# Kernel optimization log

Measured on AMD Instinct MI355X. Metric: run time of the kernel, lower is better.

Reference implementation:

```python
import jax, jax.numpy as jnp
from jax import lax
import numpy as np

N = 87296
NUM_CLASSES = 91
IOU_THRESH = 0.6
MAX_OUT = 100
IMG = 2048.0


def setup_inputs() -> dict:
    key = jax.random.key(0)
    k1, k2, k3, k4, k5 = jax.random.split(key, 5)
    class_logits = jax.random.normal(k1, (N, NUM_CLASSES), dtype=jnp.float32)
    box_regression = jax.random.normal(k2, (N, 4), dtype=jnp.float32)
    box_ctrness = jax.random.normal(k3, (N, 1), dtype=jnp.float32)
    # anchors: valid x1,y1,x2,y2 boxes inside a 2048x2048 image
    ctr = jax.random.uniform(k4, (N, 2), dtype=jnp.float32) * IMG
    wh = jax.random.uniform(k5, (N, 2), dtype=jnp.float32) * 64.0 + 8.0
    anchors = jnp.concatenate([ctr - 0.5 * wh, ctr + 0.5 * wh], axis=1)
    return {"class_logits": class_logits, "box_regression": box_regression,
            "box_ctrness": box_ctrness, "anchors": anchors}


def _decode(rel_codes, anchors):
    # torchvision BoxLinearCoder(normalize_by_size=True).decode
    ctr_x = 0.5 * (anchors[:, 0] + anchors[:, 2])
    ctr_y = 0.5 * (anchors[:, 1] + anchors[:, 3])
    w = anchors[:, 2] - anchors[:, 0]
    h = anchors[:, 3] - anchors[:, 1]
    dl = rel_codes[:, 0] * w
    dt = rel_codes[:, 1] * h
    dr = rel_codes[:, 2] * w
    db = rel_codes[:, 3] * h
    return jnp.stack([ctr_x - dl, ctr_y - dt, ctr_x + dr, ctr_y + db], axis=1)


def _nms_keep(boxes, scores, iou_thresh, max_out):
    # torchvision.ops.nms truncated to max_out; returns indices sorted by score.
    areas = jnp.maximum(boxes[:, 2] - boxes[:, 0], 0.0) * jnp.maximum(boxes[:, 3] - boxes[:, 1], 0.0)

    def body(i, state):
        cur_scores, keep = state
        idx = jnp.argmax(cur_scores)
        keep = keep.at[i].set(idx.astype(jnp.int32))
        b = boxes[idx]
        ix1 = jnp.maximum(b[0], boxes[:, 0])
        iy1 = jnp.maximum(b[1], boxes[:, 1])
        ix2 = jnp.minimum(b[2], boxes[:, 2])
        iy2 = jnp.minimum(b[3], boxes[:, 3])
        inter = jnp.maximum(ix2 - ix1, 0.0) * jnp.maximum(iy2 - iy1, 0.0)
        iou = inter / (areas[idx] + areas - inter)
        # suppress boxes with IoU > thresh (includes the selected box itself)
        cur_scores = jnp.where(iou > iou_thresh, -jnp.inf, cur_scores)
        return cur_scores, keep

    keep0 = jnp.zeros((max_out,), jnp.int32)
    _, keep = lax.fori_loop(0, max_out, body, (scores, keep0))
    return keep


def reference(class_logits, box_regression, box_ctrness, anchors):
    pred_boxes = _decode(box_regression, anchors)              # [N,4]
    cls_scores = jax.nn.sigmoid(class_logits)                  # [N,C]
    ctr_scores = jax.nn.sigmoid(box_ctrness[:, 0])             # [N]
    scores = jnp.sqrt(cls_scores * ctr_scores[:, None])        # [N,C]
    max_scores = jnp.max(scores, axis=1)                       # [N]
    labels = jnp.argmax(scores, axis=1)                        # [N]
    keep = _nms_keep(pred_boxes, max_scores, IOU_THRESH, MAX_OUT)
    return pred_boxes[keep], labels[keep], max_scores[keep]
```

## Files before the change

kernel.cpp:

```cpp
#include <hip/hip_runtime.h>
#include <math.h>

#define N_ANCH 87296
#define NCLS 91
#define NBINS 4096
#define K_CAND 256
#define CAP 512
#define MAX_OUT 100
#define IOU_TH 0.6f
#define NB1 682
#define BT1 128
#define T2 1024
#define NB16 10912


__device__ __forceinline__ float sigmoidf_(float x) {
    return 1.0f / (1.0f + expf(-x));
}

__global__ void __launch_bounds__(BT1, 4)
score_decode_kernel(const float* __restrict__ logits,
                    const float* __restrict__ boxreg,
                    const float* __restrict__ ctr,
                    const float* __restrict__ anchors,
                    unsigned short* __restrict__ bins,
                    float4* __restrict__ pbox,
                    float4* __restrict__ pmeta) {
    __shared__ float pool[2 * 16 * 91];
    const int tid  = threadIdx.x;
    const int lane = tid & 63;
    const int w    = tid >> 6;
    const int bid  = blockIdx.x;
    const int wavebase = bid * BT1 + w * 64;

    float*  buf = pool + w * 1456;
    float4* l4  = (float4*)buf;

    const int r  = lane & 15;
    const int q  = lane >> 4;
    const int q0 = q * 23;
    const int qn = (q == 3) ? 22 : 23;

    float m = -INFINITY;
    int   lab = 0;

    #pragma unroll
    for (int c = 0; c < 4; ++c) {
        const float4* g4 = (const float4*)logits +
                           ((size_t)(wavebase + c * 16) * 91) / 4;
        #pragma unroll
        for (int k = 0; k < 6; ++k) {
            int idx = k * 64 + lane;
            if (idx < 364) l4[idx] = g4[idx];
        }
        const float* rp = buf + r * 91 + q0;
        float cm = rp[0];
        int   ci = q0;
        #pragma unroll
        for (int j = 1; j < 23; ++j) {
            if (j < qn) {
                float v = rp[j];
                if (v > cm) { cm = v; ci = q0 + j; }
            }
        }
        float om = __shfl_xor(cm, 16, 64);
        int   oi = __shfl_xor(ci, 16, 64);
        if (om > cm || (om == cm && oi < ci)) { cm = om; ci = oi; }
        om = __shfl_xor(cm, 32, 64);
        oi = __shfl_xor(ci, 32, 64);
        if (om > cm || (om == cm && oi < ci)) { cm = om; ci = oi; }

        if (c == (lane >> 4)) { m = cm; lab = ci; }
    }

    const int i = wavebase + lane;
    const float s = sqrtf(sigmoidf_(m) * sigmoidf_(ctr[i]));
    const int bin = min(max((int)(s * (float)NBINS), 0), NBINS - 1);
    bins[i] = (unsigned short)bin;

    float4 A = ((const float4*)anchors)[i];
    float4 R = ((const float4*)boxreg)[i];
    float cx = 0.5f * (A.x + A.z);
    float cy = 0.5f * (A.y + A.w);
    float ww = A.z - A.x;
    float hh = A.w - A.y;
    float4 bb;
    bb.x = cx - R.x * ww;
    bb.y = cy - R.y * hh;
    bb.z = cx + R.z * ww;
    bb.w = cy + R.w * hh;
    pbox[i] = bb;
    float4 mt;
    mt.x = fmaxf(bb.z - bb.x, 0.0f) * fmaxf(bb.w - bb.y, 0.0f);
    mt.y = (float)lab;
    mt.z = s;
    mt.w = 0.0f;
    pmeta[i] = mt;
}

__global__ void __launch_bounds__(T2)
select_nms_kernel(const unsigned short* __restrict__ bins,
                  const float4* __restrict__ pbox,
                  const float4* __restrict__ pmeta,
                  float* __restrict__ out) {
    __shared__ unsigned hist[NBINS];
    __shared__ int      lidx[CAP];
    __shared__ unsigned cnt;
    __shared__ int      s_fb;
    __shared__ float    s_best[16];
    __shared__ int      s_bid[16];
    __shared__ float    s_box[5];
    __shared__ int      s_lab;

    const int tid  = threadIdx.x;
    const int lane = tid & 63;
    const int wid  = tid >> 6;

    for (int b = tid; b < NBINS; b += T2) hist[b] = 0u;
    if (tid == 0) cnt = 0u;
    __syncthreads();

    const uint4* b4 = (const uint4*)bins;
    uint4 bv[11];
    #pragma unroll
    for (int k = 0; k < 11; ++k) {
        int idx = k * T2 + tid;
        if (idx < NB16) {
            bv[k] = b4[idx];
        } else {
            uint4 z; z.x = z.y = z.z = z.w = 0u;
            bv[k] = z;
        }
    }

    #pragma unroll
    for (int k = 0; k < 11; ++k) {
        unsigned vv[4] = {bv[k].x, bv[k].y, bv[k].z, bv[k].w};
        #pragma unroll
        for (int j = 0; j < 4; ++j) {
            atomicAdd(&hist[vv[j] & 0xFFFFu], 1u);
            atomicAdd(&hist[vv[j] >> 16], 1u);
        }
    }
    __syncthreads();

    if (tid < 64) {
        const uint4* h4 = (const uint4*)hist;
        uint4 c[16];
        #pragma unroll
        for (int q = 0; q < 16; ++q) c[q] = h4[lane * 16 + q];

        unsigned local = 0;
        #pragma unroll
        for (int q = 0; q < 16; ++q) local += c[q].x + c[q].y + c[q].z + c[q].w;

        unsigned p = local;
        #pragma unroll
        for (int d = 1; d < 64; d <<= 1) {
            unsigned t = (unsigned)__shfl_down((int)p, d, 64);
            if (lane + d < 64) p += t;
        }
        unsigned long long mask = __ballot(p >= K_CAND);
        int L = 63 - __clzll(mask);
        unsigned sufAbove = (unsigned)__shfl((int)p, L + 1, 64);
        if (L == 63) sufAbove = 0u;

        if (lane == L) {
            unsigned cum = sufAbove;
            int fb = L * 64;
            bool found = false;
            #pragma unroll
            for (int q = 15; q >= 0; --q) {
                cum += c[q].w; if (!found && cum >= K_CAND) { fb = L * 64 + q * 4 + 3; found = true; }
                cum += c[q].z; if (!found && cum >= K_CAND) { fb = L * 64 + q * 4 + 2; found = true; }
                cum += c[q].y; if (!found && cum >= K_CAND) { fb = L * 64 + q * 4 + 1; found = true; }
                cum += c[q].x; if (!found && cum >= K_CAND) { fb = L * 64 + q * 4 + 0; found = true; }
            }
            s_fb = fb;
        }
    }
    __syncthreads();
    const unsigned FB = (unsigned)s_fb;

    #pragma unroll
    for (int k = 0; k < 11; ++k) {
        int idx = k * T2 + tid;
        if (idx < NB16) {
            unsigned vv[4] = {bv[k].x, bv[k].y, bv[k].z, bv[k].w};
            #pragma unroll
            for (int j = 0; j < 4; ++j) {
                unsigned lo = vv[j] & 0xFFFFu;
                unsigned hi = vv[j] >> 16;
                if (lo >= FB) {
                    unsigned pos = atomicAdd(&cnt, 1u);
                    if (pos < CAP) lidx[pos] = idx * 8 + 2 * j;
                }
                if (hi >= FB) {
                    unsigned pos = atomicAdd(&cnt, 1u);
                    if (pos < CAP) lidx[pos] = idx * 8 + 2 * j + 1;
                }
            }
        }
    }
    __syncthreads();
    const int M = (int)min(cnt, (unsigned)CAP);

    float SC, X1, Y1, X2, Y2, AR;
    int LAB;
    if (tid < M) {
        int ai = lidx[tid];
        float4 bb = pbox[ai];
        float4 mt = pmeta[ai];
        X1 = bb.x; Y1 = bb.y; X2 = bb.z; Y2 = bb.w;
        AR = mt.x;
        LAB = (int)mt.y;
        SC = mt.z;
    } else {
        SC = -INFINITY;
        X1 = Y1 = X2 = Y2 = AR = 0.0f;
        LAB = 0;
    }
    __syncthreads();

    for (int it = 0; it < MAX_OUT; ++it) {
        float b = SC;
        int id = tid;
        #pragma unroll
        for (int d = 32; d >= 1; d >>= 1) {
            float ob = __shfl_xor(b, d, 64);
            int   oid = __shfl_xor(id, d, 64);
            if (ob > b) { b = ob; id = oid; }
        }
        if (lane == 0) { s_best[wid] = b; s_bid[wid] = id; }
        __syncthreads();
        float gb = s_best[0];
        int gid = s_bid[0];
        #pragma unroll
        for (int w = 1; w < 16; ++w) {
            if (s_best[w] > gb) { gb = s_best[w]; gid = s_bid[w]; }
        }
        if (tid == gid) {
            s_box[0] = X1; s_box[1] = Y1; s_box[2] = X2; s_box[3] = Y2;
            s_box[4] = AR; s_lab = LAB;
        }
        __syncthreads();
        float sx1 = s_box[0], sy1 = s_box[1], sx2 = s_box[2], sy2 = s_box[3];
        float sar = s_box[4];
        int   slab = s_lab;

        if (tid == 0) {
            out[it * 4 + 0] = sx1;
            out[it * 4 + 1] = sy1;
            out[it * 4 + 2] = sx2;
            out[it * 4 + 3] = sy2;
            out[4 * MAX_OUT + it] = (float)slab;
            out[5 * MAX_OUT + it] = gb;
        }

        if (sar == 0.0f) {
            for (int r = it + 1 + tid; r < MAX_OUT; r += T2) {
                out[r * 4 + 0] = sx1;
                out[r * 4 + 1] = sy1;
                out[r * 4 + 2] = sx2;
                out[r * 4 + 3] = sy2;
                out[4 * MAX_OUT + r] = (float)slab;
                out[5 * MAX_OUT + r] = gb;
            }
            return;
        }

        float ix1 = fmaxf(sx1, X1);
        float iy1 = fmaxf(sy1, Y1);
        float ix2 = fminf(sx2, X2);
        float iy2 = fminf(sy2, Y2);
        float inter = fmaxf(ix2 - ix1, 0.0f) * fmaxf(iy2 - iy1, 0.0f);
        float iou = inter / (sar + AR - inter);
        if (iou > IOU_TH) SC = -INFINITY;
        __syncthreads();
    }
}

extern "C" void kernel_launch(void* const* d_in, const int* in_sizes, int n_in,
                              void* d_out, int out_size, void* d_ws, size_t ws_size,
                              hipStream_t stream) {
    const float* logits  = (const float*)d_in[0];
    const float* boxreg  = (const float*)d_in[1];
    const float* ctr     = (const float*)d_in[2];
    const float* anchors = (const float*)d_in[3];
    float* out = (float*)d_out;

    char* ws = (char*)d_ws;
    unsigned short* bins = (unsigned short*)(ws + 0);
    float4*         pbox = (float4*)(ws + 174592);
    float4*         pmeta= (float4*)(ws + 1571328);

    score_decode_kernel<<<NB1, BT1, 0, stream>>>(logits, boxreg, ctr, anchors,
                                                 bins, pbox, pmeta);
    select_nms_kernel<<<1, T2, 0, stream>>>(bins, pbox, pmeta, out);
}
```

Baseline: 30.66 us.

## Double-buffer logits via direct global-to-LDS loads and prefilter histogram with sampled threshold

The score kernel now stages logits into two LDS buffers per wave using global_load_lds, so the load of the next 16-row chunk overlaps the argmax reduction of the current one, with explicit waitcnt fences. Occupancy hint drops to 2 blocks per SM because LDS use doubles. The select kernel first builds a small histogram from a 1/16 sample to pick a conservative low threshold, then counts only bins above it into the full histogram, which cuts shared-memory atomics. A fallback pass adds the remaining bins when too few candidates pass. The extra passes and syncs add overhead, and hand-written waitcnt counts risk ordering errors.

```diff
diff --git a/kernel.cpp b/kernel.cpp
--- a/kernel.cpp
+++ b/kernel.cpp
@@ -5,6 +5,7 @@
 #define NCLS 91
 #define NBINS 4096
 #define K_CAND 256
+#define K_SAMP 8
 #define CAP 512
 #define MAX_OUT 100
 #define IOU_TH 0.6f
@@ -18,7 +19,44 @@
     return 1.0f / (1.0f + expf(-x));
 }
 
-__global__ void __launch_bounds__(BT1, 4)
+__device__ __forceinline__ void scan_thresh(const unsigned* hist, int lane,
+                                            unsigned K, int* s_dst) {
+    const uint4* h4 = (const uint4*)hist;
+    uint4 c[16];
+    #pragma unroll
+    for (int q = 0; q < 16; ++q) c[q] = h4[lane * 16 + q];
+
+    unsigned local = 0;
+    #pragma unroll
+    for (int q = 0; q < 16; ++q) local += c[q].x + c[q].y + c[q].z + c[q].w;
+
+    unsigned p = local;
+    #pragma unroll
+    for (int d = 1; d < 64; d <<= 1) {
+        unsigned t = (unsigned)__shfl_down((int)p, d, 64);
+        if (lane + d < 64) p += t;
+    }
+    unsigned long long mask = __ballot(p >= K);
+    int L = 63 - __clzll(mask);
+    unsigned sufAbove = (unsigned)__shfl((int)p, L + 1, 64);
+    if (L == 63) sufAbove = 0u;
+
+    if (lane == L) {
+        unsigned cum = sufAbove;
+        int fb = L * 64;
+        bool found = false;
+        #pragma unroll
+        for (int q = 15; q >= 0; --q) {
+            cum += c[q].w; if (!found && cum >= K) { fb = L * 64 + q * 4 + 3; found = true; }
+            cum += c[q].z; if (!found && cum >= K) { fb = L * 64 + q * 4 + 2; found = true; }
+            cum += c[q].y; if (!found && cum >= K) { fb = L * 64 + q * 4 + 1; found = true; }
+            cum += c[q].x; if (!found && cum >= K) { fb = L * 64 + q * 4 + 0; found = true; }
+        }
+        *s_dst = fb;
+    }
+}
+
+__global__ void __launch_bounds__(BT1, 2)
 score_decode_kernel(const float* __restrict__ logits,
                     const float* __restrict__ boxreg,
                     const float* __restrict__ ctr,
@@ -26,15 +64,31 @@
                     unsigned short* __restrict__ bins,
                     float4* __restrict__ pbox,
                     float4* __restrict__ pmeta) {
-    __shared__ float pool[2 * 16 * 91];
+    __shared__ __align__(16) float pool[2 * 2 * 1456];
     const int tid  = threadIdx.x;
     const int lane = tid & 63;
     const int w    = tid >> 6;
     const int bid  = blockIdx.x;
     const int wavebase = bid * BT1 + w * 64;
 
-    float*  buf = pool + w * 1456;
-    float4* l4  = (float4*)buf;
+    float* bufA = pool + w * 2912;
+    float* bufB = bufA + 1456;
+
+    const float4* g4 = (const float4*)logits + (size_t)wavebase * 91 / 4;
+
+#define STAGE(buf, c) do {                                                   \
+        const float4* gs_ = g4 + (c) * 364;                                  \
+        _Pragma("unroll")                                                    \
+        for (int k_ = 0; k_ < 6; ++k_) {                                     \
+            int idx_ = k_ * 64 + lane;                                       \
+            if (idx_ < 364) {                                                \
+                __builtin_amdgcn_global_load_lds(                            \
+                    (const __attribute__((address_space(1))) void*)(gs_ + idx_), \
+                    (__attribute__((address_space(3))) void*)((buf) + k_ * 256), \
+                    16, 0, 0);                                               \
+            }                                                                \
+        }                                                                    \
+    } while (0)
 
     const int r  = lane & 15;
     const int q  = lane >> 4;
@@ -44,34 +98,42 @@
     float m = -INFINITY;
     int   lab = 0;
 
-    #pragma unroll
-    for (int c = 0; c < 4; ++c) {
-        const float4* g4 = (const float4*)logits +
-                           ((size_t)(wavebase + c * 16) * 91) / 4;
-        #pragma unroll
-        for (int k = 0; k < 6; ++k) {
-            int idx = k * 64 + lane;
-            if (idx < 364) l4[idx] = g4[idx];
-        }
-        const float* rp = buf + r * 91 + q0;
-        float cm = rp[0];
-        int   ci = q0;
-        #pragma unroll
-        for (int j = 1; j < 23; ++j) {
-            if (j < qn) {
-                float v = rp[j];
-                if (v > cm) { cm = v; ci = q0 + j; }
-            }
-        }
-        float om = __shfl_xor(cm, 16, 64);
-        int   oi = __shfl_xor(ci, 16, 64);
-        if (om > cm || (om == cm && oi < ci)) { cm = om; ci = oi; }
-        om = __shfl_xor(cm, 32, 64);
-        oi = __shfl_xor(ci, 32, 64);
-        if (om > cm || (om == cm && oi < ci)) { cm = om; ci = oi; }
-
-        if (c == (lane >> 4)) { m = cm; lab = ci; }
-    }
+#define REDUCE(buf, c) do {                                                  \
+        const float* rp_ = (buf) + r * 91 + q0;                              \
+        float cm_ = rp_[0];                                                  \
+        int   ci_ = q0;                                                      \
+        _Pragma("unroll")                                                    \
+        for (int j_ = 1; j_ < 23; ++j_) {                                    \
+            if (j_ < qn) {                                                   \
+                float v_ = rp_[j_];                                          \
+                if (v_ > cm_) { cm_ = v_; ci_ = q0 + j_; }                   \
+            }                                                                \
+        }                                                                    \
+        float om_ = __shfl_xor(cm_, 16, 64);                                 \
+        int   oi_ = __shfl_xor(ci_, 16, 64);                                 \
+        if (om_ > cm_ || (om_ == cm_ && oi_ < ci_)) { cm_ = om_; ci_ = oi_; }\
+        om_ = __shfl_xor(cm_, 32, 64);                                       \
+        oi_ = __shfl_xor(ci_, 32, 64);                                       \
+        if (om_ > cm_ || (om_ == cm_ && oi_ < ci_)) { cm_ = om_; ci_ = oi_; }\
+        if ((c) == q) { m = cm_; lab = ci_; }                                \
+    } while (0)
+
+    STAGE(bufA, 0);
+    STAGE(bufB, 1);
+    asm volatile("s_waitcnt vmcnt(6)" ::: "memory");
+    REDUCE(bufA, 0);
+    asm volatile("s_waitcnt lgkmcnt(0)" ::: "memory");
+    STAGE(bufA, 2);
+    asm volatile("s_waitcnt vmcnt(6)" ::: "memory");
+    REDUCE(bufB, 1);
+    asm volatile("s_waitcnt lgkmcnt(0)" ::: "memory");
+    STAGE(bufB, 3);
+    asm volatile("s_waitcnt vmcnt(6)" ::: "memory");
+    REDUCE(bufA, 2);
+    asm volatile("s_waitcnt vmcnt(0)" ::: "memory");
+    REDUCE(bufB, 3);
+#undef STAGE
+#undef REDUCE
 
     const int i = wavebase + lane;
     const float s = sqrtf(sigmoidf_(m) * sigmoidf_(ctr[i]));
@@ -106,7 +168,8 @@
     __shared__ unsigned hist[NBINS];
     __shared__ int      lidx[CAP];
     __shared__ unsigned cnt;
-    __shared__ int      s_fb;
+    __shared__ int      s_tlo, s_fb;
+    __shared__ unsigned s_nf[16];
     __shared__ float    s_best[16];
     __shared__ int      s_bid[16];
     __shared__ float    s_box[5];
@@ -118,7 +181,6 @@
 
     for (int b = tid; b < NBINS; b += T2) hist[b] = 0u;
     if (tid == 0) cnt = 0u;
-    __syncthreads();
 
     const uint4* b4 = (const uint4*)bins;
     uint4 bv[11];
@@ -132,53 +194,64 @@
             bv[k] = z;
         }
     }
+    __syncthreads();
 
     #pragma unroll
     for (int k = 0; k < 11; ++k) {
-        unsigned vv[4] = {bv[k].x, bv[k].y, bv[k].z, bv[k].w};
+        int idx = k * T2 + tid;
+        if (idx < NB16 && (idx & 7) == 0)
+            atomicAdd(&hist[bv[k].x & 0xFFFFu], 1u);
+    }
+    __syncthreads();
+    if (tid < 64) scan_thresh(hist, lane, K_SAMP, &s_tlo);
+    __syncthreads();
+    const unsigned TLO = (unsigned)s_tlo;
+
+    for (int b = tid; b < NBINS; b += T2) hist[b] = 0u;
+    __syncthreads();
+
+    unsigned nf = 0;
+    #pragma unroll
+    for (int k = 0; k < 11; ++k) {
+        int idx = k * T2 + tid;
+        if (idx < NB16) {
+            unsigned vv[4] = {bv[k].x, bv[k].y, bv[k].z, bv[k].w};
+            #pragma unroll
+            for (int j = 0; j < 4; ++j) {
+                unsigned lo = vv[j] & 0xFFFFu;
+                unsigned hi = vv[j] >> 16;
+                if (lo >= TLO) { atomicAdd(&hist[lo], 1u); ++nf; }
+                if (hi >= TLO) { atomicAdd(&hist[hi], 1u); ++nf; }
+            }
+        }
+    }
+    #pragma unroll
+    for (int d = 32; d >= 1; d >>= 1)
+        nf += (unsigned)__shfl_down((int)nf, d, 64);
+    if (lane == 0) s_nf[wid] = nf;
+    __syncthreads();
+    unsigned NF = 0;
+    #pragma unroll
+    for (int ww = 0; ww < 16; ++ww) NF += s_nf[ww];
+
+    if (NF < K_CAND) {
         #pragma unroll
-        for (int j = 0; j < 4; ++j) {
-            atomicAdd(&hist[vv[j] & 0xFFFFu], 1u);
-            atomicAdd(&hist[vv[j] >> 16], 1u);
-        }
-    }
-    __syncthreads();
-
-    if (tid < 64) {
-        const uint4* h4 = (const uint4*)hist;
-        uint4 c[16];
-        #pragma unroll
-        for (int q = 0; q < 16; ++q) c[q] = h4[lane * 16 + q];
-
-        unsigned local = 0;
-        #pragma unroll
-        for (int q = 0; q < 16; ++q) local += c[q].x + c[q].y + c[q].z + c[q].w;
-
-        unsigned p = local;
-        #pragma unroll
-        for (int d = 1; d < 64; d <<= 1) {
-            unsigned t = (unsigned)__shfl_down((int)p, d, 64);
-            if (lane + d < 64) p += t;
-        }
-        unsigned long long mask = __ballot(p >= K_CAND);
-        int L = 63 - __clzll(mask);
-        unsigned sufAbove = (unsigned)__shfl((int)p, L + 1, 64);
-        if (L == 63) sufAbove = 0u;
-
-        if (lane == L) {
-            unsigned cum = sufAbove;
-            int fb = L * 64;
-            bool found = false;
-            #pragma unroll
-            for (int q = 15; q >= 0; --q) {
-                cum += c[q].w; if (!found && cum >= K_CAND) { fb = L * 64 + q * 4 + 3; found = true; }
-                cum += c[q].z; if (!found && cum >= K_CAND) { fb = L * 64 + q * 4 + 2; found = true; }
-                cum += c[q].y; if (!found && cum >= K_CAND) { fb = L * 64 + q * 4 + 1; found = true; }
-                cum += c[q].x; if (!found && cum >= K_CAND) { fb = L * 64 + q * 4 + 0; found = true; }
+        for (int k = 0; k < 11; ++k) {
+            int idx = k * T2 + tid;
+            if (idx < NB16) {
+                unsigned vv[4] = {bv[k].x, bv[k].y, bv[k].z, bv[k].w};
+                #pragma unroll
+                for (int j = 0; j < 4; ++j) {
+                    unsigned lo = vv[j] & 0xFFFFu;
+                    unsigned hi = vv[j] >> 16;
+                    if (lo < TLO) atomicAdd(&hist[lo], 1u);
+                    if (hi < TLO) atomicAdd(&hist[hi], 1u);
+                }
             }
-            s_fb = fb;
-        }
-    }
+        }
+    }
+    __syncthreads();
+    if (tid < 64) scan_thresh(hist, lane, K_CAND, &s_fb);
     __syncthreads();
     const unsigned FB = (unsigned)s_fb;
 
```

After: 30.74 us. No clear change (+0.3%).
